# Optimization experiments

Hardware: AMD Instinct MI355X
Metric: run time of the kernel (lower is better)

Reference implementation:

```python
import jax, jax.numpy as jnp
import numpy as np

SUBBOX_SCORE_THRESH = 0.1
NMS_IOU_THRESH = 0.5
LEGACY_BBOX = False
MAX_BOX_NUM = 32
ROI_WH_ZOOM_SCALE = (1.0, 1.0)
CLASS_OFFSET = 4096.0  # > max possible box coordinate; separates classes for class-aware NMS


def setup_inputs() -> dict:
    key = jax.random.key(0)
    k1, k2, k3, k4 = jax.random.split(key, 4)
    B, N, C, H, W = 8, 256, 8, 16, 16
    # valid rois: x1<x2, y1<y2
    xy = jax.random.uniform(k1, (B, N, 2), minval=0.0, maxval=800.0)
    wh = jax.random.uniform(k2, (B, N, 2), minval=16.0, maxval=256.0)
    rois = jnp.concatenate([xy, xy + wh], axis=-1)
    rcnn_cls_pred = jax.random.uniform(k3, (B * N, C, H, W), dtype=jnp.float32)
    rcnn_reg_pred = jax.random.normal(k4, (B * N, 4, H, W), dtype=jnp.float32) * 0.5
    return {"rois": rois, "rcnn_cls_pred": rcnn_cls_pred, "rcnn_reg_pred": rcnn_reg_pred}


def _iou_matrix(boxes):
    off = 1.0 if LEGACY_BBOX else 0.0
    x1, y1, x2, y2 = boxes[:, 0], boxes[:, 1], boxes[:, 2], boxes[:, 3]
    area = jnp.clip(x2 - x1 + off, 0.0) * jnp.clip(y2 - y1 + off, 0.0)
    ix1 = jnp.maximum(x1[:, None], x1[None, :])
    iy1 = jnp.maximum(y1[:, None], y1[None, :])
    ix2 = jnp.minimum(x2[:, None], x2[None, :])
    iy2 = jnp.minimum(y2[:, None], y2[None, :])
    inter = jnp.clip(ix2 - ix1 + off, 0.0) * jnp.clip(iy2 - iy1 + off, 0.0)
    union = area[:, None] + area[None, :] - inter
    return inter / jnp.maximum(union, 1e-9)


def _nms_single(boxes, scores, labels):
    # boxes [M,4], scores [M], labels [M] (shared) -> padded keep of size MAX_BOX_NUM
    M = boxes.shape[0]
    K = MAX_BOX_NUM
    valid = scores >= SUBBOX_SCORE_THRESH
    order = jnp.argsort(-scores)
    b = boxes[order]
    s = scores[order]
    l = labels[order]
    v = valid[order]
    # class-aware NMS: offset coordinates per class so boxes of different classes never overlap
    ob = b + (l.astype(b.dtype) * CLASS_OFFSET)[:, None]
    iou = jax.lax.stop_gradient(_iou_matrix(ob))
    ar = jnp.arange(M)

    def body(i, sup):
        keep_i = v[i] & jnp.logical_not(sup[i])
        return sup | (keep_i & (iou[i] > NMS_IOU_THRESH) & (ar > i))

    sup = jax.lax.fori_loop(0, M, body, jnp.zeros((M,), bool))
    keep = v & jnp.logical_not(sup)
    rank = jnp.cumsum(keep) - 1
    slot = jnp.where(keep & (rank < K), rank, K)  # overflow/invalid -> dummy slot K
    out_b = jnp.zeros((K + 1, 4), b.dtype).at[slot].set(b)[:K]
    out_s = jnp.zeros((K + 1,), s.dtype).at[slot].set(s)[:K]
    out_l = jnp.full((K + 1,), -1, jnp.int32).at[slot].set(l.astype(jnp.int32))[:K]
    return out_b, out_s, out_l


def _decode(rois, cls_pred, reg_pred):
    B, N, _ = rois.shape
    BN = B * N
    _, C, H, W = cls_pred.shape
    r = rois.reshape(BN, 4)
    # zoom_boxes: scale w/h about box center
    sx, sy = ROI_WH_ZOOM_SCALE
    cx = (r[:, 0] + r[:, 2]) * 0.5
    cy = (r[:, 1] + r[:, 3]) * 0.5
    rw = (r[:, 2] - r[:, 0]) * sx
    rh = (r[:, 3] - r[:, 1]) * sy
    rx1 = cx - rw * 0.5
    ry1 = cy - rh * 0.5
    bsw = (rw / W)[:, None, None, None]  # [BN,1,1,1]
    bsh = (rh / H)[:, None, None, None]
    rx1b = rx1[:, None, None, None]
    ry1b = ry1[:, None, None, None]
    ind_w = jnp.arange(W, dtype=cls_pred.dtype)            # broadcasts over last (w) axis
    ind_h = jnp.arange(H, dtype=cls_pred.dtype)[:, None]   # broadcasts over h axis
    ox1 = reg_pred[:, 0][:, None]  # [BN,1,H,W] -- identical for every class
    oy1 = reg_pred[:, 1][:, None]
    ox2 = reg_pred[:, 2][:, None]
    oy2 = reg_pred[:, 3][:, None]
    bx1 = bsw * (ox1 + ind_w + 0.5) + rx1b
    by1 = bsh * (oy1 + ind_h + 0.5) + ry1b
    bx2 = bsw * (ox2 + ind_w + 0.5) + rx1b
    by2 = bsh * (oy2 + ind_h + 0.5) + ry1b
    mask = cls_pred > SUBBOX_SCORE_THRESH  # [BN,C,H,W]
    z = jnp.zeros((), cls_pred.dtype)
    scores = jnp.where(mask, cls_pred, z).reshape(BN, C, H * W)
    K = MAX_BOX_NUM
    top_s, top_i = jax.lax.top_k(scores, K)  # [BN,C,K]

    def gather(bm):
        bm = jnp.where(mask, bm, z).reshape(BN, C, H * W)
        return jnp.take_along_axis(bm, top_i, axis=-1)

    boxes = jnp.stack([gather(bx1), gather(by1), gather(bx2), gather(by2)], axis=-1)  # [BN,C,K,4]
    M = C * K
    boxes = boxes.reshape(BN, M, 4)
    res_scores = top_s.reshape(BN, M)
    labels = jnp.broadcast_to(jnp.arange(C)[:, None], (C, K)).reshape(M)
    nb, ns, nl = jax.vmap(_nms_single, in_axes=(0, 0, None))(boxes, res_scores, labels)
    return nb.reshape(B, N, K, 4), ns.reshape(B, N, K), nl.reshape(B, N, K)


def reference(rois, rcnn_cls_pred, rcnn_reg_pred):
    # Returns padded per-roi NMS results: boxes [B,N,K,4], scores [B,N,K], labels [B,N,K]
    # (labels == -1 and scores == 0 mark padded slots)
    return _decode(rois, rcnn_cls_pred, rcnn_reg_pred)
```

## Files before the change

kernel.cpp:

```cpp
#include <hip/hip_runtime.h>

#define NCLS   8
#define HW     256
#define KOUT   32
#define SCORE_T 0.1f

typedef unsigned long long u64;
typedef unsigned int u32;

template<int CTRL>
__device__ __forceinline__ u32 dpp32(u32 x) {
  return (u32)__builtin_amdgcn_mov_dpp((int)x, CTRL, 0xF, 0xF, false);
}
template<int ST>
__device__ __forceinline__ u32 lxor32(u32 x) {
  if constexpr (ST == 1 || ST == 2 || ST == 8) {
    constexpr int C = (ST == 1) ? 0xB1 : (ST == 2) ? 0x4E : 0x128;
    return dpp32<C>(x);
  } else if constexpr (ST == 4) {
    return dpp32<0x1B>(dpp32<0x141>(x));
  } else {
    return __shfl_xor(x, ST, 64);
  }
}
template<int ST>
__device__ __forceinline__ u32 ce32(u32 v, bool up, int lane) {
  u32 o = lxor32<ST>(v);
  bool keepMax = (up == ((lane & ST) == 0));
  return ((v > o) == keepMax) ? v : o;
}
__device__ __forceinline__ void cepair(u32 &a, u32 &b) {
  const u32 mx = (a > b) ? a : b;
  const u32 mn = (a > b) ? b : a;
  a = mx; b = mn;
}

__device__ __forceinline__ void wave_top32x2(u32 v[8], int lane) {
  const bool u2 = (lane & 2) == 0;
  const bool u4 = (lane & 4) == 0;
  const bool u8 = (lane & 8) == 0;
  #define ALL8(ST, UP) { v[0]=ce32<ST>(v[0],UP,lane); v[1]=ce32<ST>(v[1],UP,lane); \
    v[2]=ce32<ST>(v[2],UP,lane); v[3]=ce32<ST>(v[3],UP,lane); \
    v[4]=ce32<ST>(v[4],UP,lane); v[5]=ce32<ST>(v[5],UP,lane); \
    v[6]=ce32<ST>(v[6],UP,lane); v[7]=ce32<ST>(v[7],UP,lane); }
  ALL8(1, u2)
  ALL8(2, u4) ALL8(1, u4)
  ALL8(4, u8) ALL8(2, u8) ALL8(1, u8)
  #define SZ16(ST) { v[0]=ce32<ST>(v[0],true,lane); v[1]=ce32<ST>(v[1],false,lane); \
    v[2]=ce32<ST>(v[2],true,lane); v[3]=ce32<ST>(v[3],false,lane); \
    v[4]=ce32<ST>(v[4],true,lane); v[5]=ce32<ST>(v[5],false,lane); \
    v[6]=ce32<ST>(v[6],true,lane); v[7]=ce32<ST>(v[7],false,lane); }
  SZ16(8) SZ16(4) SZ16(2) SZ16(1)
  cepair(v[0], v[1]); cepair(v[2], v[3]); cepair(v[4], v[5]); cepair(v[6], v[7]);
  ALL8(8, true) ALL8(4, true) ALL8(2, true) ALL8(1, true)
  #undef ALL8
  #undef SZ16
  { u32 o;
    o = dpp32<0x140>(v[3]); v[0] = (v[0] > o) ? v[0] : o;
    o = dpp32<0x140>(v[2]); v[1] = (v[1] > o) ? v[1] : o;
    o = dpp32<0x140>(v[7]); v[4] = (v[4] > o) ? v[4] : o;
    o = dpp32<0x140>(v[6]); v[5] = (v[5] > o) ? v[5] : o; }
  #define CL4(ST) { v[0]=ce32<ST>(v[0],true,lane); v[1]=ce32<ST>(v[1],true,lane); \
                    v[4]=ce32<ST>(v[4],true,lane); v[5]=ce32<ST>(v[5],true,lane); }
  cepair(v[0], v[1]); cepair(v[4], v[5]);
  CL4(8) CL4(4) CL4(2) CL4(1)
  const int pm = 15 - (lane & 15);
  const int permC = ((lane ^ 16) & 48) | pm;
  { u32 oa = __shfl(v[1], permC, 64);
    u32 ob = __shfl(v[0], permC, 64);
    u32 oc = __shfl(v[5], permC, 64);
    u32 od = __shfl(v[4], permC, 64);
    v[0] = (v[0] > oa) ? v[0] : oa;
    v[1] = (v[1] > ob) ? v[1] : ob;
    v[4] = (v[4] > oc) ? v[4] : oc;
    v[5] = (v[5] > od) ? v[5] : od; }
  cepair(v[0], v[1]); cepair(v[4], v[5]);
  CL4(8) CL4(4) CL4(2) CL4(1)
  const int permD = ((lane ^ 32) & 48) | pm;
  { u32 oa = __shfl(v[1], permD, 64);
    u32 ob = __shfl(v[0], permD, 64);
    u32 oc = __shfl(v[5], permD, 64);
    u32 od = __shfl(v[4], permD, 64);
    v[0] = (v[0] > oa) ? v[0] : oa;
    v[1] = (v[1] > ob) ? v[1] : ob;
    v[4] = (v[4] > oc) ? v[4] : oc;
    v[5] = (v[5] > od) ? v[5] : od; }
  cepair(v[0], v[1]); cepair(v[4], v[5]);
  CL4(8) CL4(4) CL4(2) CL4(1)
  #undef CL4
}

__device__ __forceinline__ u32 wave_merge8_32(u32 v[4], int lane) {
  #define MSTAGET(ST) { \
    v[0]=ce32<ST>(v[0],true,lane); v[1]=ce32<ST>(v[1],true,lane); \
    v[2]=ce32<ST>(v[2],true,lane); v[3]=ce32<ST>(v[3],true,lane); }
  #pragma unroll
  for (int r = 0; r < 4; ++r) {
    u32 o = __shfl_xor(v[r], 63, 64);
    u32 mx = (v[r] > o) ? v[r] : o;
    u32 mn = (v[r] > o) ? o : v[r];
    v[r] = (lane < 32) ? mx : mn;
  }
  MSTAGET(16) MSTAGET(8) MSTAGET(4) MSTAGET(2) MSTAGET(1)
  { u32 o1 = __shfl_xor(v[1], 31, 64); v[0] = (v[0] > o1) ? v[0] : o1;
    u32 o3 = __shfl_xor(v[3], 31, 64); v[2] = (v[2] > o3) ? v[2] : o3; }
  v[0]=ce32<16>(v[0],true,lane); v[2]=ce32<16>(v[2],true,lane);
  v[0]=ce32<8>(v[0],true,lane);  v[2]=ce32<8>(v[2],true,lane);
  v[0]=ce32<4>(v[0],true,lane);  v[2]=ce32<4>(v[2],true,lane);
  v[0]=ce32<2>(v[0],true,lane);  v[2]=ce32<2>(v[2],true,lane);
  v[0]=ce32<1>(v[0],true,lane);  v[2]=ce32<1>(v[2],true,lane);
  { u32 o2 = __shfl_xor(v[2], 31, 64); v[0] = (v[0] > o2) ? v[0] : o2; }
  v[0]=ce32<16>(v[0],true,lane); v[0]=ce32<8>(v[0],true,lane);
  v[0]=ce32<4>(v[0],true,lane);  v[0]=ce32<2>(v[0],true,lane);
  v[0]=ce32<1>(v[0],true,lane);
  #undef MSTAGET
  return v[0];
}

__global__ __launch_bounds__(256) void decode_nms_kernel(
    const float* __restrict__ rois,
    const float* __restrict__ cls,
    const float* __restrict__ reg,
    float* __restrict__ out,
    int BN)
{
  const int bn   = blockIdx.x;
  const int tid  = threadIdx.x;
  const int lane = tid & 63;
  const int wave = tid >> 6;

  __shared__ float4 sbox[HW];
  __shared__ u32 ck[NCLS * KOUT];
  __shared__ float sq_x1[NCLS * KOUT], sq_y1[NCLS * KOUT];
  __shared__ float sq_x2[NCLS * KOUT], sq_y2[NCLS * KOUT];
  __shared__ float sq_ar[NCLS * KOUT];
  __shared__ u32 mk2[NCLS * KOUT];
  __shared__ u32 idxt[NCLS * KOUT];

  mk2[tid] = 0u;

  const float r0 = rois[bn * 4 + 0];
  const float r1 = rois[bn * 4 + 1];
  const float r2 = rois[bn * 4 + 2];
  const float r3 = rois[bn * 4 + 3];
  const float cx  = (r0 + r2) * 0.5f;
  const float cy  = (r1 + r3) * 0.5f;
  const float rw  = (r2 - r0) * 1.0f;
  const float rh  = (r3 - r1) * 1.0f;
  const float rx1 = cx - rw * 0.5f;
  const float ry1 = cy - rh * 0.5f;
  const float bsw = rw / 16.0f;
  const float bsh = rh / 16.0f;

  const float* clsb = cls + (size_t)bn * (NCLS * HW);
  u32 v[8];
  #pragma unroll
  for (int q = 0; q < 2; ++q) {
    const int c = (wave << 1) | q;
    #pragma unroll
    for (int r = 0; r < 4; ++r) {
      const int e = (lane & 15) | ((r & 1) << 4) | ((r >> 1) << 5)
                  | ((lane >> 4) << 6);
      const float s   = clsb[c * HW + e];
      const float msv = (s > SCORE_T) ? s : 0.0f;
      const u32 mk = (u32)(msv * 8388608.0f);
      v[q * 4 + r] = (mk << 8) | (u32)(255 - e);
    }
  }

  {
    const int w = tid & 15, h2 = tid >> 4;
    const float ox1 = reg[bn * 1024 +   0 + tid];
    const float oy1 = reg[bn * 1024 + 256 + tid];
    const float ox2 = reg[bn * 1024 + 512 + tid];
    const float oy2 = reg[bn * 1024 + 768 + tid];
    const float tx1 = (ox1 + (float)w) + 0.5f;
    const float ty1 = (oy1 + (float)h2) + 0.5f;
    const float tx2 = (ox2 + (float)w) + 0.5f;
    const float ty2 = (oy2 + (float)h2) + 0.5f;
    sbox[tid] = make_float4(__fadd_rn(__fmul_rn(bsw, tx1), rx1),
                            __fadd_rn(__fmul_rn(bsh, ty1), ry1),
                            __fadd_rn(__fmul_rn(bsw, tx2), rx1),
                            __fadd_rn(__fmul_rn(bsh, ty2), ry1));
  }

  wave_top32x2(v, lane);
  if (lane < 16) {
    const int cA = (wave << 1), cB = cA | 1;
    ck[(cA << 5) | lane]        = v[0];
    ck[(cA << 5) | 16 | lane]   = v[1];
    ck[(cB << 5) | lane]        = v[4];
    ck[(cB << 5) | 16 | lane]   = v[5];
  }
  __syncthreads();

  const int j  = lane & 31;
  const int h  = lane >> 5;
  const int cc = (wave << 1) | h;
  const u32 myk = ck[(cc << 5) + j];
  const u32 mk  = myk >> 8;
  const int idx = 255 - (int)(myk & 255u);
  const bool valid = (mk >= 838861u);

  const float off = 4096.0f * (float)cc;
  const float4 bx = valid ? sbox[idx] : make_float4(0.f, 0.f, 0.f, 0.f);
  const float obx1 = bx.x + off;
  const float oby1 = bx.y + off;
  const float obx2 = bx.z + off;
  const float oby2 = bx.w + off;
  const float ar = __fmul_rn(fmaxf(obx2 - obx1, 0.0f),
                             fmaxf(oby2 - oby1, 0.0f));

  const int row = (cc << 5) | j;
  sq_x1[row] = obx1; sq_y1[row] = oby1;
  sq_x2[row] = obx2; sq_y2[row] = oby2;
  sq_ar[row] = ar;

  unsigned ov = 0u;
  #pragma unroll
  for (int k = 0; k < 16; ++k) {
    const int pk = (j + 1 + k) & 31;
    const int rr = (cc << 5) | pk;
    const float px1 = sq_x1[rr], py1 = sq_y1[rr];
    const float px2 = sq_x2[rr], py2 = sq_y2[rr];
    const float ia  = sq_ar[rr];
    const float xx1 = fmaxf(px1, obx1);
    const float yy1 = fmaxf(py1, oby1);
    const float xx2 = fminf(px2, obx2);
    const float yy2 = fminf(py2, oby2);
    const float iw  = fmaxf(xx2 - xx1, 0.0f);
    const float ih  = fmaxf(yy2 - yy1, 0.0f);
    const float inter = __fmul_rn(iw, ih);
    const float uni   = fmaxf(__fsub_rn(__fadd_rn(ia, ar), inter), 1e-9f);
    const double di = (double)inter * 33554432.0;
    const double du = (double)uni   * 16777217.0;
    ov |= (di > du) ? (1u << pk) : 0u;
  }

  u64 keep = __ballot(valid);
  #pragma unroll
  for (int i = 0; i < 32; ++i) {
    const u64 colb = __ballot(((ov >> i) & 1u) != 0u);
    const u32 rA = (u32)__builtin_amdgcn_readlane((int)ov, i);
    const u32 rB = (u32)__builtin_amdgcn_readlane((int)ov, i + 32);
    const u64 col = colb | (u64)rA | ((u64)rB << 32);
    const unsigned jm = 0xFFFFFFFEu << i;
    const u64 jmask = ((u64)jm << 32) | (u64)jm;
    const u64 mlo = (0ull - ((keep >> i) & 1ull)) & 0x00000000FFFFFFFFull;
    const u64 mhi = (0ull - ((keep >> (i + 32)) & 1ull)) << 32;
    keep &= ~(col & jmask & (mlo | mhi));
  }

  const unsigned kh = (unsigned)(keep >> (h << 5));
  const int rank = __popc(kh & ((1u << j) - 1u));
  if ((kh >> j) & 1u) {
    mk2[(cc << 5) + rank]  = (mk << 8) | (u32)((7 - cc) << 5) | (u32)(31 - rank);
    idxt[(cc << 5) + rank] = (u32)idx;
  }
  __syncthreads();

  if (wave == 0) {
    u32 w4[4];
    #pragma unroll
    for (int r = 0; r < 4; ++r) w4[r] = mk2[(r << 6) | lane];
    const u32 f = wave_merge8_32(w4, lane);

    float* ob = out + (size_t)bn * (KOUT * 4);
    float* os = out + (size_t)BN * (KOUT * 4) + (size_t)bn * KOUT;
    float* ol = out + (size_t)BN * (KOUT * 5) + (size_t)bn * KOUT;
    if (lane < KOUT) {
      if (f != 0u) {
        const u32  fm  = f >> 8;
        const float sc = (float)fm * 1.1920928955078125e-7f;
        const int  ccf = 7 - (int)((f >> 5) & 7u);
        const int  rkf = 31 - (int)(f & 31u);
        const int  ii  = (int)idxt[(ccf << 5) + rkf];
        const float4 b = sbox[ii];
        ob[lane * 4 + 0] = b.x;
        ob[lane * 4 + 1] = b.y;
        ob[lane * 4 + 2] = b.z;
        ob[lane * 4 + 3] = b.w;
        os[lane] = sc;
        ol[lane] = (float)ccf;
      } else {
        ob[lane * 4 + 0] = 0.0f;
        ob[lane * 4 + 1] = 0.0f;
        ob[lane * 4 + 2] = 0.0f;
        ob[lane * 4 + 3] = 0.0f;
        os[lane] = 0.0f;
        ol[lane] = -1.0f;
      }
    }
  }
}

extern "C" void kernel_launch(void* const* d_in, const int* in_sizes, int n_in,
                              void* d_out, int out_size, void* d_ws, size_t ws_size,
                              hipStream_t stream) {
  const float* rois = (const float*)d_in[0];
  const float* cls  = (const float*)d_in[1];
  const float* reg  = (const float*)d_in[2];
  float* out = (float*)d_out;
  const int BN = in_sizes[0] / 4;
  decode_nms_kernel<<<dim3(BN), dim3(256), 0, stream>>>(rois, cls, reg, out, BN);
}
```

Before: 25.20 us.

## Prefilter scores by fixed threshold and bitonic-sort survivors for per-class top-32

Each wave compacts candidate keys above a fixed high-score threshold into shared memory using ballot and mbcnt. When both of its classes have between 32 and 64 survivors, it runs a 64-element bitonic sort instead of the full top-32 network over all 256 values. Otherwise it falls back to the original top-32 routine, which also gains an extra merge stage. The fast path only pays off when the score distribution puts enough elements above the threshold, and it adds LDS traffic, ballots and a divergent branch.

```diff
diff --git a/kernel.cpp b/kernel.cpp
--- a/kernel.cpp
+++ b/kernel.cpp
@@ -33,6 +33,18 @@
   const u32 mx = (a > b) ? a : b;
   const u32 mn = (a > b) ? b : a;
   a = mx; b = mn;
+}
+
+__device__ __forceinline__ void wave_sort64x2_desc(u32 &a, u32 &b, int lane) {
+  #define SS(SZ, ST) { const bool up_ = ((lane & (SZ)) == 0); \
+    a = ce32<ST>(a, up_, lane); b = ce32<ST>(b, up_, lane); }
+  SS(2,1)
+  SS(4,2)  SS(4,1)
+  SS(8,4)  SS(8,2)  SS(8,1)
+  SS(16,8) SS(16,4) SS(16,2) SS(16,1)
+  SS(32,16) SS(32,8) SS(32,4) SS(32,2) SS(32,1)
+  SS(64,32) SS(64,16) SS(64,8) SS(64,4) SS(64,2) SS(64,1)
+  #undef SS
 }
 
 __device__ __forceinline__ void wave_top32x2(u32 v[8], int lane) {
@@ -46,6 +58,7 @@
   ALL8(1, u2)
   ALL8(2, u4) ALL8(1, u4)
   ALL8(4, u8) ALL8(2, u8) ALL8(1, u8)
+  ALL8(8, (lane & 16) == 0) ALL8(4, (lane & 16) == 0) ALL8(2, (lane & 16) == 0) ALL8(1, (lane & 16) == 0)
   #define SZ16(ST) { v[0]=ce32<ST>(v[0],true,lane); v[1]=ce32<ST>(v[1],false,lane); \
     v[2]=ce32<ST>(v[2],true,lane); v[3]=ce32<ST>(v[3],false,lane); \
     v[4]=ce32<ST>(v[4],true,lane); v[5]=ce32<ST>(v[5],false,lane); \
@@ -136,6 +149,7 @@
   __shared__ float sq_ar[NCLS * KOUT];
   __shared__ u32 mk2[NCLS * KOUT];
   __shared__ u32 idxt[NCLS * KOUT];
+  __shared__ u32 cbuf[4][2][64];
 
   mk2[tid] = 0u;
 
@@ -161,9 +175,8 @@
     for (int r = 0; r < 4; ++r) {
       const int e = (lane & 15) | ((r & 1) << 4) | ((r >> 1) << 5)
                   | ((lane >> 4) << 6);
-      const float s   = clsb[c * HW + e];
-      const float msv = (s > SCORE_T) ? s : 0.0f;
-      const u32 mk = (u32)(msv * 8388608.0f);
+      const float s = clsb[c * HW + e];
+      const u32 mk = (u32)(s * 8388608.0f);
       v[q * 4 + r] = (mk << 8) | (u32)(255 - e);
     }
   }
@@ -184,13 +197,45 @@
                             __fadd_rn(__fmul_rn(bsh, ty2), ry1));
   }
 
-  wave_top32x2(v, lane);
-  if (lane < 16) {
-    const int cA = (wave << 1), cB = cA | 1;
-    ck[(cA << 5) | lane]        = v[0];
-    ck[(cA << 5) | 16 | lane]   = v[1];
-    ck[(cB << 5) | lane]        = v[4];
-    ck[(cB << 5) | 16 | lane]   = v[5];
+  const u32 T0KEY = (6794772u << 8) | 255u;
+  cbuf[wave][0][lane] = 0u;
+  cbuf[wave][1][lane] = 0u;
+  u32 cnt0, cnt1;
+  #pragma unroll
+  for (int q = 0; q < 2; ++q) {
+    u32 base = 0;
+    #pragma unroll
+    for (int r = 0; r < 4; ++r) {
+      const u32 key = v[q * 4 + r];
+      const bool surv = key > T0KEY;
+      const u64 bal = __ballot(surv);
+      const u32 pos = __builtin_amdgcn_mbcnt_hi((u32)(bal >> 32),
+                      __builtin_amdgcn_mbcnt_lo((u32)bal, 0u));
+      const u32 rank = base + pos;
+      if (surv && rank < 64u) cbuf[wave][q][rank] = key;
+      base += (u32)__popcll(bal);
+    }
+    if (q == 0) cnt0 = base; else cnt1 = base;
+  }
+  const bool fast = (cnt0 >= 32u) & (cnt0 <= 64u)
+                  & (cnt1 >= 32u) & (cnt1 <= 64u);
+  if (fast) {
+    u32 a = cbuf[wave][0][lane];
+    u32 b = cbuf[wave][1][lane];
+    wave_sort64x2_desc(a, b, lane);
+    if (lane < 32) {
+      ck[(((wave << 1)    ) << 5) | lane] = a;
+      ck[(((wave << 1) | 1) << 5) | lane] = b;
+    }
+  } else {
+    wave_top32x2(v, lane);
+    if (lane < 16) {
+      const int cA = (wave << 1), cB = cA | 1;
+      ck[(cA << 5) | lane]      = v[0];
+      ck[(cA << 5) | 16 | lane] = v[1];
+      ck[(cB << 5) | lane]      = v[4];
+      ck[(cB << 5) | 16 | lane] = v[5];
+    }
   }
   __syncthreads();
 
```

After: 24.49 us. 1.03x faster.
